# Kernel tuning notes

Measured on AMD Instinct MI355X. Metric: run time of the kernel, lower is better.

The kernel has to match this reference:

```python
import jax, jax.numpy as jnp
import numpy as np

SEQ_LEN, BATCH, VOCAB = 128, 32, 32000
EMB, HID = 32, 16


def setup_inputs() -> dict:
    key = jax.random.key(0)
    ks = jax.random.split(key, 10)
    return {
        "input_batch": jax.random.randint(ks[0], (SEQ_LEN, BATCH), 0, VOCAB, dtype=jnp.int64)
        if jax.config.jax_enable_x64 else jax.random.randint(ks[0], (SEQ_LEN, BATCH), 0, VOCAB, dtype=jnp.int32),
        "h0_lr": jax.random.uniform(ks[1], (BATCH, HID), dtype=jnp.float32),
        "h0_rl": jax.random.uniform(ks[2], (BATCH, HID), dtype=jnp.float32),
        "embedding": jax.random.normal(ks[3], (VOCAB, EMB), dtype=jnp.float32),
        "W_lr": jax.random.normal(ks[4], (HID, EMB + HID), dtype=jnp.float32) * 0.25,
        "b_lr": jax.random.normal(ks[5], (HID,), dtype=jnp.float32) * 0.25,
        "W_rl": jax.random.normal(ks[6], (HID, EMB + HID), dtype=jnp.float32) * 0.25,
        "b_rl": jax.random.normal(ks[7], (HID,), dtype=jnp.float32) * 0.25,
        "W_ho": jax.random.normal(ks[8], (VOCAB, 2 * HID), dtype=jnp.float32) * 0.25,
        "b_ho": jax.random.normal(ks[9], (VOCAB,), dtype=jnp.float32) * 0.25,
    }


def _rnn_step(W, b):
    # h_{t+1} = tanh([x_t, h_t] @ W^T + b)
    def f(h, x):
        h_new = jnp.tanh(jnp.concatenate([x, h], axis=-1) @ W.T + b)
        return h_new, h_new
    return f


def reference(input_batch, h0_lr, h0_rl, embedding, W_lr, b_lr, W_rl, b_rl, W_ho, b_ho):
    emb = embedding[input_batch]  # [S, B, EMB]
    # Left-to-right: consumes emb[0..S-2]; hLR[0] = h0_lr, len S
    _, hs_lr = jax.lax.scan(_rnn_step(W_lr, b_lr), h0_lr, emb[:-1])
    hLR = jnp.concatenate([h0_lr[None], hs_lr], axis=0)  # [S, B, HID]
    # Right-to-left: consumes emb[S-1 .. 1]; hRL[0] = h0_rl, len S
    _, hs_rl = jax.lax.scan(_rnn_step(W_rl, b_rl), h0_rl, emb[:0:-1])
    hRL = jnp.concatenate([h0_rl[None], hs_rl], axis=0)  # [S, B, HID]
    # prediction[i] pairs hLR[i] with hRL[S-1-i]
    combined = jnp.concatenate([hLR, hRL[::-1]], axis=-1)  # [S, B, 2*HID]
    logits = combined @ W_ho.T + b_ho  # [S, B, VOCAB]
    return jax.nn.log_softmax(logits, axis=-1)
```

## Files before the change

### kernel.cpp

```cpp
#include <hip/hip_runtime.h>
#include <hip/hip_bf16.h>
#include <math.h>

#define SS 128
#define BB 32
#define VV 32000
#define EE 32
#define HH 16
#define KK 32
#define NROWS (SS*BB)
#define NSL 16
#define VT 125
#define NPRE 8
#define WSL 80
#define WVT 25

typedef __attribute__((ext_vector_type(4))) float f32x4;
typedef __attribute__((ext_vector_type(8))) short bf16x8;
typedef __attribute__((ext_vector_type(4))) short s16x4;

#define DPPF(x, ctrl) __builtin_bit_cast(float, __builtin_amdgcn_update_dpp( \
    __builtin_bit_cast(int, (x)), __builtin_bit_cast(int, (x)), (ctrl), 0xF, 0xF, false))

__global__ __launch_bounds__(256) void k_prep(
    const float* __restrict__ Who, __hip_bfloat16* __restrict__ who_bf,
    const int* __restrict__ tok, const float* __restrict__ emb,
    const float* __restrict__ Wlr, const float* __restrict__ blr,
    const float* __restrict__ Wrl, const float* __restrict__ brl,
    float* __restrict__ xp) {
  if (blockIdx.x < 1000) {
    int i = blockIdx.x * 256 + threadIdx.x;
    f32x4 v = ((const f32x4*)Who)[i];
    s16x4 o;
    #pragma unroll
    for (int q = 0; q < 4; ++q) {
      __hip_bfloat16 h = __float2bfloat16(v[q]);
      o[q] = *reinterpret_cast<short*>(&h);
    }
    ((s16x4*)who_bf)[i] = o;
  } else {
    int g = (blockIdx.x - 1000) * 256 + threadIdx.x;
    int dir = g >> 16;
    int rem = g & 65535;
    int t = rem >> 9;
    int b = (rem >> 4) & 31;
    int j = rem & 15;
    const float* W  = dir ? Wrl : Wlr;
    const float* bv = dir ? brl : blr;
    int tk = tok[t*BB + b];
    const float* er = emb + tk*EE;
    const float* wr = W + j*(EE+HH);
    float acc = bv[j];
    #pragma unroll
    for (int k = 0; k < EE; ++k) acc += er[k] * wr[k];
    xp[g] = acc;
  }
}

__global__ __launch_bounds__(128) void k_rnn_fused(
    const float* __restrict__ xp,
    const float* __restrict__ h0lr, const float* __restrict__ h0rl,
    const float* __restrict__ Wlr, const float* __restrict__ Wrl,
    __hip_bfloat16* __restrict__ comb_bf) {
  int bid = blockIdx.x;
  int dir = bid >> 2;
  int b = (bid & 3) * 8 + (threadIdx.x >> 4);
  int j = threadIdx.x & 15;
  const float* W  = dir ? Wrl : Wlr;
  const float* h0 = dir ? h0rl : h0lr;
  float wr[HH];
  #pragma unroll
  for (int r = 0; r < HH; ++r) wr[r] = W[j*(EE+HH) + EE + (j ^ r)];
  const float* x = xp + dir * (SS*BB*HH);
  int u = b*HH + j;
  float h = h0[u];
  if (dir == 0) comb_bf[0*(BB*KK) + b*KK + j] = __float2bfloat16(h);
  else          comb_bf[(SS-1)*(BB*KK) + b*KK + HH + j] = __float2bfloat16(h);
  float xbuf[NPRE];
  #pragma unroll
  for (int p = 0; p < NPRE; ++p) {
    int tt = 1 + p;
    int off = dir ? (SS-tt)*(BB*HH) + u : (tt-1)*(BB*HH) + u;
    xbuf[p] = x[off];
  }
  for (int tc = 1; tc < SS; tc += NPRE) {
    #pragma unroll
    for (int i = 0; i < NPRE; ++i) {
      int t = tc + i;
      if (t < SS) {
        float xv = xbuf[i];
        int tp = t + NPRE;
        int offp = (tp < SS) ? (dir ? (SS-tp)*(BB*HH) + u : (tp-1)*(BB*HH) + u) : u;
        xbuf[i] = x[offp];
        float t1  = DPPF(h, 0xB1);
        float t2  = DPPF(h, 0x4E);
        float t3  = DPPF(h, 0x1B);
        float t7  = DPPF(h, 0x141);
        float t15 = DPPF(h, 0x140);
        float t4  = DPPF(t7, 0x1B);
        float t5  = DPPF(t7, 0x4E);
        float t6  = DPPF(t7, 0xB1);
        float t8  = DPPF(t15, 0x141);
        float t12 = DPPF(t15, 0x1B);
        float t13 = DPPF(t15, 0x4E);
        float t14 = DPPF(t15, 0xB1);
        float t9  = DPPF(t8, 0xB1);
        float t10 = DPPF(t8, 0x4E);
        float t11 = DPPF(t8, 0x1B);
        float a0 = fmaf(wr[0], h,  xv);
        a0 = fmaf(wr[4],  t4,  a0);
        a0 = fmaf(wr[8],  t8,  a0);
        a0 = fmaf(wr[12], t12, a0);
        float a1 = wr[1] * t1;
        a1 = fmaf(wr[5],  t5,  a1);
        a1 = fmaf(wr[9],  t9,  a1);
        a1 = fmaf(wr[13], t13, a1);
        float a2 = wr[2] * t2;
        a2 = fmaf(wr[6],  t6,  a2);
        a2 = fmaf(wr[10], t10, a2);
        a2 = fmaf(wr[14], t14, a2);
        float a3 = wr[3] * t3;
        a3 = fmaf(wr[7],  t7,  a3);
        a3 = fmaf(wr[11], t11, a3);
        a3 = fmaf(wr[15], t15, a3);
        float acc = (a0 + a1) + (a2 + a3);
        float e = __expf(2.f * acc);
        h = fmaf(-2.f, __builtin_amdgcn_rcpf(e + 1.f), 1.f);
        int ci = dir ? ((SS-1-t)*(BB*KK) + b*KK + HH + j)
                     : (t*(BB*KK) + b*KK + j);
        comb_bf[ci] = __float2bfloat16(h);
      }
    }
  }
}

__global__ __launch_bounds__(256) void k_sumexp(
    const __hip_bfloat16* __restrict__ cb, const __hip_bfloat16* __restrict__ wb,
    const float* __restrict__ bho, float* __restrict__ part) {
  int wg = ((blockIdx.x & 7) << 7) | (blockIdx.x >> 3);
  int w = wg * 4 + (threadIdx.x >> 6);
  int lane = threadIdx.x & 63;
  int rt = w >> 4;
  int sl = w & 15;
  int v0 = sl * (VT*16);
  int g = lane >> 4, c = lane & 15;
  bf16x8 bfr = *(const bf16x8*)(cb + (size_t)(rt*16 + c)*KK + g*8);
  float s = 0.f;
  for (int t = 0; t < VT; ++t) {
    int v = v0 + t*16;
    bf16x8 af = *(const bf16x8*)(wb + (size_t)(v + c)*KK + g*8);
    f32x4 bh = *(const f32x4*)(bho + v + g*4);
    f32x4 d = __builtin_amdgcn_mfma_f32_16x16x32_bf16(af, bfr, bh, 0, 0, 0);
    s += __expf(d[0]) + __expf(d[1]) + __expf(d[2]) + __expf(d[3]);
  }
  s += __shfl_xor(s, 16);
  s += __shfl_xor(s, 32);
  if (lane < 16)
    part[(size_t)(rt*16 + lane)*NSL + sl] = s;
}

__global__ __launch_bounds__(256) void k_write(
    const __hip_bfloat16* __restrict__ cb, const __hip_bfloat16* __restrict__ wb,
    const float* __restrict__ bho, const float* __restrict__ part,
    float* __restrict__ out) {
  __shared__ char afl[WVT * 1024];
  __shared__ float bhl[WVT * 16];
  int bid = blockIdx.x;
  int wg = ((bid & 7) * 640) + (bid >> 3);
  int rtg = wg / WSL;
  int sl  = wg % WSL;
  int v0  = sl * (WVT*16);
  int tid = threadIdx.x;
  const f32x4* src = (const f32x4*)(wb + (size_t)v0 * KK);
  for (int o = tid; o < WVT*64; o += 256) {
    f32x4 v = src[o];
    int t = o >> 6, u = o & 63;
    int us = u ^ ((u >> 3) & 7);
    *(f32x4*)(afl + t*1024 + us*16) = v;
  }
  for (int o = tid; o < WVT*16; o += 256) bhl[o] = bho[v0 + o];
  __syncthreads();
  int wid = tid >> 6, lane = tid & 63;
  int rt = rtg*4 + wid;
  int g = lane >> 4, c = lane & 15;
  size_t row = (size_t)rt*16 + c;
  const f32x4* pp = (const f32x4*)(part + row*NSL);
  f32x4 p0 = pp[0], p1 = pp[1], p2 = pp[2], p3 = pp[3];
  float s = (p0[0]+p0[1]+p0[2]+p0[3]) + (p1[0]+p1[1]+p1[2]+p1[3])
          + (p2[0]+p2[1]+p2[2]+p2[3]) + (p3[0]+p3[1]+p3[2]+p3[3]);
  float Lr = logf(s);
  bf16x8 bfr = *(const bf16x8*)(cb + row*KK + g*8);
  int u = c*4 + g;
  int us = u ^ ((u >> 3) & 7);
  const char* afp = afl + us*16;
  float* op = out + row*VV + v0 + g*4;
  for (int t = 0; t < WVT; ++t) {
    bf16x8 a = *(const bf16x8*)(afp + t*1024);
    f32x4 bh = *(const f32x4*)(bhl + t*16 + g*4);
    f32x4 cin = bh - Lr;
    f32x4 d = __builtin_amdgcn_mfma_f32_16x16x32_bf16(a, bfr, cin, 0, 0, 0);
    *(f32x4*)(op + t*16) = d;
  }
}

extern "C" void kernel_launch(void* const* d_in, const int* in_sizes, int n_in,
                              void* d_out, int out_size, void* d_ws, size_t ws_size,
                              hipStream_t stream) {
  const int*   tok  = (const int*)d_in[0];
  const float* h0lr = (const float*)d_in[1];
  const float* h0rl = (const float*)d_in[2];
  const float* emb  = (const float*)d_in[3];
  const float* Wlr  = (const float*)d_in[4];
  const float* blr  = (const float*)d_in[5];
  const float* Wrl  = (const float*)d_in[6];
  const float* brl  = (const float*)d_in[7];
  const float* Who  = (const float*)d_in[8];
  const float* bho  = (const float*)d_in[9];
  float* out = (float*)d_out;
  float* ws  = (float*)d_ws;

  float* xp   = ws;
  float* part = ws + 131072;
  __hip_bfloat16* comb_bf = (__hip_bfloat16*)(ws + 196608);
  __hip_bfloat16* who_bf  = (__hip_bfloat16*)(ws + 262144);

  hipLaunchKernelGGL(k_prep, dim3(1512), dim3(256), 0, stream,
                     Who, who_bf, tok, emb, Wlr, blr, Wrl, brl, xp);
  hipLaunchKernelGGL(k_rnn_fused, dim3(8), dim3(128), 0, stream,
                     xp, h0lr, h0rl, Wlr, Wrl, comb_bf);
  hipLaunchKernelGGL(k_sumexp, dim3(1024), dim3(256), 0, stream,
                     comb_bf, who_bf, bho, part);
  hipLaunchKernelGGL(k_write, dim3(5120), dim3(256), 0, stream,
                     comb_bf, who_bf, bho, part, out);
}
```

Before: 193.3 us.

## Stage RNN inputs in LDS and load output weights directly into registers

The RNN kernel now copies all of its block's precomputed input projections into shared memory up front with vectorized loads, replacing the per-step global prefetch ring with LDS reads. The logits-write kernel no longer stages weight and bias tiles through LDS behind a barrier. Each wave instead loads its 25 weight fragments and bias vectors straight into registers before issuing the MFMAs. The aim is to shorten the serial RNN's global-latency exposure and to remove the LDS round trip and barrier in the write kernel, at the cost of a large LDS footprint and higher register pressure.

Result: slower. 203.0 us (+5.0%).

```diff
diff --git a/kernel.cpp b/kernel.cpp
--- a/kernel.cpp
+++ b/kernel.cpp
@@ -11,7 +11,6 @@
 #define NROWS (SS*BB)
 #define NSL 16
 #define VT 125
-#define NPRE 8
 #define WSL 80
 #define WVT 25
 
@@ -62,75 +61,74 @@
     const float* __restrict__ h0lr, const float* __restrict__ h0rl,
     const float* __restrict__ Wlr, const float* __restrict__ Wrl,
     __hip_bfloat16* __restrict__ comb_bf) {
+  __shared__ float xl[127*128];
   int bid = blockIdx.x;
   int dir = bid >> 2;
-  int b = (bid & 3) * 8 + (threadIdx.x >> 4);
-  int j = threadIdx.x & 15;
+  int tid = threadIdx.x;
+  int b = (bid & 3) * 8 + (tid >> 4);
+  int j = tid & 15;
   const float* W  = dir ? Wrl : Wlr;
   const float* h0 = dir ? h0rl : h0lr;
   float wr[HH];
   #pragma unroll
   for (int r = 0; r < HH; ++r) wr[r] = W[j*(EE+HH) + EE + (j ^ r)];
-  const float* x = xp + dir * (SS*BB*HH);
+  {
+    const float* xbase = xp + dir * (SS*BB*HH) + (bid & 3) * (8*HH);
+    for (int o = tid; o < 127*32; o += 128) {
+      int r = o >> 5, q = o & 31;
+      int grow = dir ? (SS-1-r) : r;
+      f32x4 v = *(const f32x4*)(xbase + grow*(BB*HH) + q*4);
+      *(f32x4*)(xl + r*128 + q*4) = v;
+    }
+  }
   int u = b*HH + j;
   float h = h0[u];
   if (dir == 0) comb_bf[0*(BB*KK) + b*KK + j] = __float2bfloat16(h);
   else          comb_bf[(SS-1)*(BB*KK) + b*KK + HH + j] = __float2bfloat16(h);
-  float xbuf[NPRE];
-  #pragma unroll
-  for (int p = 0; p < NPRE; ++p) {
-    int tt = 1 + p;
-    int off = dir ? (SS-tt)*(BB*HH) + u : (tt-1)*(BB*HH) + u;
-    xbuf[p] = x[off];
-  }
-  for (int tc = 1; tc < SS; tc += NPRE) {
-    #pragma unroll
-    for (int i = 0; i < NPRE; ++i) {
-      int t = tc + i;
-      if (t < SS) {
-        float xv = xbuf[i];
-        int tp = t + NPRE;
-        int offp = (tp < SS) ? (dir ? (SS-tp)*(BB*HH) + u : (tp-1)*(BB*HH) + u) : u;
-        xbuf[i] = x[offp];
-        float t1  = DPPF(h, 0xB1);
-        float t2  = DPPF(h, 0x4E);
-        float t3  = DPPF(h, 0x1B);
-        float t7  = DPPF(h, 0x141);
-        float t15 = DPPF(h, 0x140);
-        float t4  = DPPF(t7, 0x1B);
-        float t5  = DPPF(t7, 0x4E);
-        float t6  = DPPF(t7, 0xB1);
-        float t8  = DPPF(t15, 0x141);
-        float t12 = DPPF(t15, 0x1B);
-        float t13 = DPPF(t15, 0x4E);
-        float t14 = DPPF(t15, 0xB1);
-        float t9  = DPPF(t8, 0xB1);
-        float t10 = DPPF(t8, 0x4E);
-        float t11 = DPPF(t8, 0x1B);
-        float a0 = fmaf(wr[0], h,  xv);
-        a0 = fmaf(wr[4],  t4,  a0);
-        a0 = fmaf(wr[8],  t8,  a0);
-        a0 = fmaf(wr[12], t12, a0);
-        float a1 = wr[1] * t1;
-        a1 = fmaf(wr[5],  t5,  a1);
-        a1 = fmaf(wr[9],  t9,  a1);
-        a1 = fmaf(wr[13], t13, a1);
-        float a2 = wr[2] * t2;
-        a2 = fmaf(wr[6],  t6,  a2);
-        a2 = fmaf(wr[10], t10, a2);
-        a2 = fmaf(wr[14], t14, a2);
-        float a3 = wr[3] * t3;
-        a3 = fmaf(wr[7],  t7,  a3);
-        a3 = fmaf(wr[11], t11, a3);
-        a3 = fmaf(wr[15], t15, a3);
-        float acc = (a0 + a1) + (a2 + a3);
-        float e = __expf(2.f * acc);
-        h = fmaf(-2.f, __builtin_amdgcn_rcpf(e + 1.f), 1.f);
-        int ci = dir ? ((SS-1-t)*(BB*KK) + b*KK + HH + j)
-                     : (t*(BB*KK) + b*KK + j);
-        comb_bf[ci] = __float2bfloat16(h);
-      }
-    }
+  __syncthreads();
+  float xr0 = xl[0*128 + tid];
+  float xr1 = xl[1*128 + tid];
+  for (int t = 1; t < SS; ++t) {
+    float xv = xr0;
+    xr0 = xr1;
+    xr1 = (t+1 < SS) ? xl[(t+1)*128 + tid] : 0.f;
+    float t1  = DPPF(h, 0xB1);
+    float t2  = DPPF(h, 0x4E);
+    float t3  = DPPF(h, 0x1B);
+    float t7  = DPPF(h, 0x141);
+    float t15 = DPPF(h, 0x140);
+    float t4  = DPPF(t7, 0x1B);
+    float t5  = DPPF(t7, 0x4E);
+    float t6  = DPPF(t7, 0xB1);
+    float t8  = DPPF(t15, 0x141);
+    float t12 = DPPF(t15, 0x1B);
+    float t13 = DPPF(t15, 0x4E);
+    float t14 = DPPF(t15, 0xB1);
+    float t9  = DPPF(t8, 0xB1);
+    float t10 = DPPF(t8, 0x4E);
+    float t11 = DPPF(t8, 0x1B);
+    float a0 = fmaf(wr[0], h,  xv);
+    a0 = fmaf(wr[4],  t4,  a0);
+    a0 = fmaf(wr[8],  t8,  a0);
+    a0 = fmaf(wr[12], t12, a0);
+    float a1 = wr[1] * t1;
+    a1 = fmaf(wr[5],  t5,  a1);
+    a1 = fmaf(wr[9],  t9,  a1);
+    a1 = fmaf(wr[13], t13, a1);
+    float a2 = wr[2] * t2;
+    a2 = fmaf(wr[6],  t6,  a2);
+    a2 = fmaf(wr[10], t10, a2);
+    a2 = fmaf(wr[14], t14, a2);
+    float a3 = wr[3] * t3;
+    a3 = fmaf(wr[7],  t7,  a3);
+    a3 = fmaf(wr[11], t11, a3);
+    a3 = fmaf(wr[15], t15, a3);
+    float acc = (a0 + a1) + (a2 + a3);
+    float e = __expf(2.f * acc);
+    h = fmaf(-2.f, __builtin_amdgcn_rcpf(e + 1.f), 1.f);
+    int ci = dir ? ((SS-1-t)*(BB*KK) + b*KK + HH + j)
+                 : (t*(BB*KK) + b*KK + j);
+    comb_bf[ci] = __float2bfloat16(h);
   }
 }
 
@@ -163,23 +161,12 @@
     const __hip_bfloat16* __restrict__ cb, const __hip_bfloat16* __restrict__ wb,
     const float* __restrict__ bho, const float* __restrict__ part,
     float* __restrict__ out) {
-  __shared__ char afl[WVT * 1024];
-  __shared__ float bhl[WVT * 16];
   int bid = blockIdx.x;
   int wg = ((bid & 7) * 640) + (bid >> 3);
   int rtg = wg / WSL;
   int sl  = wg % WSL;
   int v0  = sl * (WVT*16);
   int tid = threadIdx.x;
-  const f32x4* src = (const f32x4*)(wb + (size_t)v0 * KK);
-  for (int o = tid; o < WVT*64; o += 256) {
-    f32x4 v = src[o];
-    int t = o >> 6, u = o & 63;
-    int us = u ^ ((u >> 3) & 7);
-    *(f32x4*)(afl + t*1024 + us*16) = v;
-  }
-  for (int o = tid; o < WVT*16; o += 256) bhl[o] = bho[v0 + o];
-  __syncthreads();
   int wid = tid >> 6, lane = tid & 63;
   int rt = rtg*4 + wid;
   int g = lane >> 4, c = lane & 15;
@@ -190,15 +177,20 @@
           + (p2[0]+p2[1]+p2[2]+p2[3]) + (p3[0]+p3[1]+p3[2]+p3[3]);
   float Lr = logf(s);
   bf16x8 bfr = *(const bf16x8*)(cb + row*KK + g*8);
-  int u = c*4 + g;
-  int us = u ^ ((u >> 3) & 7);
-  const char* afp = afl + us*16;
+  bf16x8 afr[WVT];
+  f32x4  cin[WVT];
+  #pragma unroll
+  for (int t = 0; t < WVT; ++t) {
+    int v = v0 + t*16;
+    afr[t] = *(const bf16x8*)(wb + (size_t)(v + c)*KK + g*8);
+    cin[t] = *(const f32x4*)(bho + v + g*4);
+  }
+  #pragma unroll
+  for (int t = 0; t < WVT; ++t) cin[t] = cin[t] - Lr;
   float* op = out + row*VV + v0 + g*4;
+  #pragma unroll
   for (int t = 0; t < WVT; ++t) {
-    bf16x8 a = *(const bf16x8*)(afp + t*1024);
-    f32x4 bh = *(const f32x4*)(bhl + t*16 + g*4);
-    f32x4 cin = bh - Lr;
-    f32x4 d = __builtin_amdgcn_mfma_f32_16x16x32_bf16(a, bfr, cin, 0, 0, 0);
+    f32x4 d = __builtin_amdgcn_mfma_f32_16x16x32_bf16(afr[t], bfr, cin[t], 0, 0, 0);
     *(f32x4*)(op + t*16) = d;
   }
 }
```
